# Kernel tuning notes

Hardware: AMD Instinct MI355X
Metric: run time of the kernel (lower is better)

The kernel has to match this reference:

```python
import jax, jax.numpy as jnp
import numpy as np

B, L, D = 4, 2048, 1024
N, K, H = 8, 1, 128
FG, FA = 4096, 2048
SEP = 1792
SOFTCAP = 50.0
EPS = 1e-6
BIG_NEG = -2.3819763e38


def setup_inputs() -> dict:
    key = jax.random.key(0)
    ks = jax.random.split(key, 16)
    def rnd(k, shape, s=0.02):
        return jax.random.normal(k, shape, dtype=jnp.float32) * s
    return {
        "x": rnd(ks[0], (B, L, D), 1.0),
        "positions": jnp.broadcast_to(jnp.arange(L + 1, dtype=jnp.int32), (B, L + 1)),
        "attn_mask": jnp.ones((B, 1, L, L), dtype=bool),
        "separation_idx": SEP,
        "pre_attn_scale": rnd(ks[1], (D,), 0.1),
        "pre_ffw_scale": rnd(ks[2], (D,), 0.1),
        "g_qw": rnd(ks[3], (N, D, H)),
        "g_kvw": rnd(ks[4], (2, K, D, H)),
        "g_ow": rnd(ks[5], (N, H, D)),
        "a_qw": rnd(ks[6], (N, D, H)),
        "a_kvw": rnd(ks[7], (2, K, D, H)),
        "a_ow": rnd(ks[8], (N, H, D)),
        "g_gate": rnd(ks[9], (2, D, FG)),
        "g_lin": rnd(ks[10], (FG, D)),
        "a_gate": rnd(ks[11], (2, D, FA)),
        "a_lin": rnd(ks[12], (FA, D)),
    }


def rms_norm(x, scale):
    var = jnp.mean(jnp.square(x), axis=-1, keepdims=True)
    return x * jax.lax.rsqrt(var + EPS) * (1.0 + scale)


def apply_rope(x, positions, max_wavelength=10_000.0):
    # x: [B,T,n,H], positions: [B,T]
    hd = x.shape[-1]
    frac = 2.0 * jnp.arange(hd // 2, dtype=jnp.float32) / hd
    timescale = max_wavelength ** frac  # [H/2]
    radians = positions.astype(jnp.float32)[:, :, None, None] / timescale  # [B,T,1,H/2]
    sin, cos = jnp.sin(radians), jnp.cos(radians)
    x1, x2 = jnp.split(x, 2, axis=-1)
    return jnp.concatenate([x1 * cos - x2 * sin, x2 * cos + x1 * sin], axis=-1).astype(x.dtype)


def get_qkv(xn, pos, qw, kvw):
    q = jnp.einsum('btd,ndh->btnh', xn, qw)
    q = apply_rope(q, pos) * (H ** -0.5)  # query_pre_attn_norm == 'rsqrt_head_dim'
    k = apply_rope(jnp.einsum('btd,kdh->btkh', xn, kvw[0]), pos)
    v = jnp.einsum('btd,kdh->btkh', xn, kvw[1])
    return q, k, v


def attention(q, k, v, mask):
    b, t, n, h = q.shape
    kk = k.shape[2]
    g = n // kk
    qg = q.reshape(b, t, kk, g, h)
    logits = jnp.einsum('btkgh,bskh->bkgts', qg, k)
    logits = SOFTCAP * jnp.tanh(logits / SOFTCAP)
    logits = jnp.where(mask[:, :, None], logits, BIG_NEG)  # mask [B,1,T,S] -> [B,1,1,T,S]
    probs = jax.nn.softmax(logits.astype(jnp.float32), axis=-1).astype(q.dtype)
    return jnp.einsum('bkgts,bskh->btkgh', probs, v).reshape(b, t, n, h)


def ffn(x, gate, lin):
    h = jax.nn.gelu(jnp.einsum('btd,df->btf', x, gate[0])) * jnp.einsum('btd,df->btf', x, gate[1])
    return jnp.einsum('btf,fd->btd', h, lin)


def process(attn_out, residual, ffw_scale, gate, lin):
    # post_norms=False, dropout=0: out = mlp(norm(attn + res)) + res (per source)
    h = rms_norm(attn_out + residual, ffw_scale)
    return ffn(h, gate, lin) + residual


def reference(x, positions, attn_mask, separation_idx, pre_attn_scale, pre_ffw_scale,
              g_qw, g_kvw, g_ow, a_qw, a_kvw, a_ow, g_gate, g_lin, a_gate, a_lin):
    sep = separation_idx
    x_g, x_a = x[:, :sep], x[:, sep:]
    n_g = rms_norm(x_g, pre_attn_scale)
    n_a = rms_norm(x_a, pre_attn_scale)
    p_g = positions[:, :sep]
    p_a = positions[:, sep + 1:]
    qg, kg, vg = get_qkv(n_g, p_g, g_qw, g_kvw)
    qa, ka, va = get_qkv(n_a, p_a, a_qw, a_kvw)
    q = jnp.concatenate([qg, qa], axis=1)
    k = jnp.concatenate([kg, ka], axis=1)
    v = jnp.concatenate([vg, va], axis=1)
    attn = attention(q, k, v, attn_mask)  # [B,L,N,H]
    go = jnp.einsum('btnh,nhd->btd', attn[:, :sep], g_ow)
    ao = jnp.einsum('btnh,nhd->btd', attn[:, sep:], a_ow)
    out_g = process(go, x_g, pre_ffw_scale, g_gate, g_lin)
    out_a = process(ao, x_a, pre_ffw_scale, a_gate, a_lin)
    return jnp.concatenate([out_g, out_a], axis=1)
```

## Files before the change

### kernel.cpp

```cpp
#include <hip/hip_runtime.h>
#include <hip/hip_bf16.h>
#include <stdint.h>

typedef short s8b __attribute__((ext_vector_type(8)));
typedef float f4 __attribute__((ext_vector_type(4)));
typedef unsigned short u16t;
typedef unsigned int u32t;

#define AS1 __attribute__((address_space(1)))
#define AS3 __attribute__((address_space(3)))
#define DEVFN static __device__ __forceinline__

DEVFN u16t f2b(float f){ union{ __hip_bfloat16 h; u16t u; } c; c.h = __float2bfloat16(f); return c.u; }

DEVFN float geluf(float x){
  float t = 0.7978845608028654f*(x + 0.044715f*x*x*x);
  t = fminf(fmaxf(t, -15.0f), 15.0f);
  float e = __expf(2.0f*t);
  return 0.5f*x*(1.0f + (e-1.0f)*__builtin_amdgcn_rcpf(e+1.0f));
}
DEVFN float softcapf(float x){
  float t = fminf(fmaxf(x*0.02f, -15.0f), 15.0f);
  float e = __expf(2.0f*t);
  return 50.0f*(e-1.0f)*__builtin_amdgcn_rcpf(e+1.0f);
}

__global__ __launch_bounds__(256) void tpack_k(u16t* __restrict__ dst, const float* __restrict__ src,
                                               int ldsrc, int lddst, int rmul, int roff, int prow,
                                               size_t pstride){
  __shared__ float tile[32][33];
  int z = blockIdx.z;
  const float* s = src + (size_t)z*pstride;
  int f0 = blockIdx.x*32, d0 = blockIdx.y*32;
  int t = threadIdx.x, r = t>>5, c = t&31;
  #pragma unroll
  for(int i=0;i<4;i++)
    tile[r + i*8][c] = s[(size_t)(d0 + r + i*8)*ldsrc + f0 + c];
  __syncthreads();
  int rbase = roff + z*prow;
  #pragma unroll
  for(int i=0;i<4;i++){
    int f = f0 + r + i*8;
    dst[(size_t)(f*rmul + rbase)*lddst + d0 + c] = f2b(tile[c][r + i*8]);
  }
}

__global__ __launch_bounds__(256) void rmsnorm_k(const float* __restrict__ x, const float* __restrict__ sc,
                                                 u16t* __restrict__ out){
  int row = blockIdx.x;
  int tid = threadIdx.x;
  const float* xr = x + (size_t)row*1024;
  float4 v = *(const float4*)(xr + tid*4);
  float s = v.x*v.x + v.y*v.y + v.z*v.z + v.w*v.w;
  #pragma unroll
  for(int off=32; off>=1; off>>=1) s += __shfl_down(s, off);
  __shared__ float ws4[4];
  if((tid & 63) == 0) ws4[tid>>6] = s;
  __syncthreads();
  float tot = ws4[0]+ws4[1]+ws4[2]+ws4[3];
  float r = rsqrtf(tot*(1.0f/1024.0f) + 1e-6f);
  float4 scv = *(const float4*)(sc + tid*4);
  u16t o0 = f2b(v.x*r*(1.0f+scv.x)), o1 = f2b(v.y*r*(1.0f+scv.y));
  u16t o2 = f2b(v.z*r*(1.0f+scv.z)), o3 = f2b(v.w*r*(1.0f+scv.w));
  uint2 pk; pk.x = (u32t)o0 | ((u32t)o1<<16); pk.y = (u32t)o2 | ((u32t)o3<<16);
  *(uint2*)(out + (size_t)row*1024 + tid*4) = pk;
}

__global__ __launch_bounds__(256) void rope_k(const float* __restrict__ qkv, u16t* __restrict__ qb,
                                              u16t* __restrict__ kswz, u16t* __restrict__ vrow){
  int row = blockIdx.x;
  int b = row >> 11, t = row & 2047;
  float pos = (float)(t + (t >= 1792 ? 1 : 0));
  const float* src = qkv + (size_t)row*1280;
  size_t kvbase = ((size_t)b*2048 + t)*128;
  int swz = ((t&7)<<3) ^ (((t>>3)&3)<<4);
  for(int idx = threadIdx.x; idx < 704; idx += 256){
    if(idx < 512){
      int n = idx >> 6, i = idx & 63;
      float inv = exp2f((float)i * -0.20762050593046f);
      float sn, cs; sincosf(pos*inv, &sn, &cs);
      float x1 = src[n*128+i], x2 = src[n*128+i+64];
      const float qs = 0.08838834764831845f;
      qb[(size_t)row*1024 + n*128 + i]      = f2b((x1*cs - x2*sn)*qs);
      qb[(size_t)row*1024 + n*128 + i + 64] = f2b((x2*cs + x1*sn)*qs);
    } else if(idx < 576){
      int i = idx - 512;
      float inv = exp2f((float)i * -0.20762050593046f);
      float sn, cs; sincosf(pos*inv, &sn, &cs);
      float x1 = src[1024+i], x2 = src[1024+i+64];
      kswz[kvbase + (i ^ swz)]        = f2b(x1*cs - x2*sn);
      kswz[kvbase + ((i+64) ^ swz)]   = f2b(x2*cs + x1*sn);
    } else {
      int h = idx - 576;
      vrow[kvbase + h] = f2b(src[1152+h]);
    }
  }
}

__global__ __launch_bounds__(256) void vt_pack_k(const u16t* __restrict__ vrow, u16t* __restrict__ vtswz){
  int blk = blockIdx.x;
  int b = blk >> 5, kt = blk & 31;
  int tid = threadIdx.x;
  const u16t* src = vrow + ((size_t)b*2048 + kt*64)*128;
  #pragma unroll
  for(int it=0; it<4; ++it){
    int o = it*2048 + tid*8;
    int d = o >> 6, kg = o & 63;
    u16t tmp[8];
    #pragma unroll
    for(int j=0;j<8;j++) tmp[j] = src[(size_t)(kg+j)*128 + d];
    *(uint4*)&vtswz[((size_t)b*128 + d)*2048 + kt*64 + (kg ^ ((d&7)<<3))] = *(const uint4*)tmp;
  }
}

struct GemmArgs {
  const u16t* A; int lda;
  const u16t* Bg; const u16t* Ba;
  int K; int ntN; int mode; int amap; int omap; int ep;
  float* outf; u16t* outb; int ldo;
  const float* res;
};

__global__ __launch_bounds__(256) void gemm_k(GemmArgs g){
  __shared__ __align__(16) u16t As[2*128*32];
  __shared__ __align__(16) u16t Bs[2*128*32];
  int bid = blockIdx.x;
  int mt = bid / g.ntN, nt = bid % g.ntN;
  int c0 = mt*128, g0;
  const u16t* B;
  if(g.mode == 0){
    g0 = c0;
    B = ((mt & 15) < 14) ? g.Bg : g.Ba;
  } else if(g.mode == 1){
    int bb = mt/14, t = (mt - bb*14)*128;
    g0 = bb*2048 + t; B = g.Bg;
  } else {
    int bb = mt>>1, t = 1792 + (mt&1)*128;
    g0 = bb*2048 + t; B = g.Bg;
  }
  int arow = g.amap ? g0 : c0;
  int orow = g.omap ? g0 : c0;
  int tid = threadIdx.x, lane = tid & 63, w = tid >> 6, l15 = lane & 15, lg = lane >> 4;
  int wr = w >> 1, wc = w & 1;

  int gsrc = ((tid&3) ^ ((tid>>3)&3))*8;
  const u16t* Ap = g.A + (size_t)(arow + (tid>>2))*g.lda + gsrc;
  const u16t* Bp = B   + (size_t)(nt*128 + (tid>>2))*g.K + gsrc;
  size_t lda64 = (size_t)64*g.lda, ldb64 = (size_t)64*g.K;
  u32t le = tid*8;

  int xr = (lg ^ ((l15>>1)&3))*8;
  int aoff[4], boff[4];
  #pragma unroll
  for(int mi=0;mi<4;mi++) aoff[mi] = (wr*64 + mi*16 + l15)*32 + xr;
  #pragma unroll
  for(int ni=0;ni<4;ni++) boff[ni] = (wc*64 + ni*16 + l15)*32 + xr;

  f4 acc[4][4];
  #pragma unroll
  for(int mi=0;mi<4;mi++)
    #pragma unroll
    for(int ni=0;ni<4;ni++){ f4 z = {0.0f,0.0f,0.0f,0.0f}; acc[mi][ni]=z; }

  auto stagef = [&](int buf, int k0){
    u16t* a = As + buf*4096;
    u16t* b = Bs + buf*4096;
    __builtin_amdgcn_global_load_lds((const AS1 u32t*)(Ap + k0),          (AS3 u32t*)&a[le],        16,0,0);
    __builtin_amdgcn_global_load_lds((const AS1 u32t*)(Ap + k0 + lda64),  (AS3 u32t*)&a[le + 2048], 16,0,0);
    __builtin_amdgcn_global_load_lds((const AS1 u32t*)(Bp + k0),          (AS3 u32t*)&b[le],        16,0,0);
    __builtin_amdgcn_global_load_lds((const AS1 u32t*)(Bp + k0 + ldb64),  (AS3 u32t*)&b[le + 2048], 16,0,0);
  };

  stagef(0, 0);
  __syncthreads();
  int cur = 0;
  for(int k0=0; k0 < g.K; k0 += 32){
    if(k0 + 32 < g.K) stagef(cur^1, k0+32);
    const u16t* as = As + cur*4096;
    const u16t* bs = Bs + cur*4096;
    s8b af[4], bf[4];
    #pragma unroll
    for(int mi=0;mi<4;mi++) af[mi] = *(const s8b*)&as[aoff[mi]];
    #pragma unroll
    for(int ni=0;ni<4;ni++) bf[ni] = *(const s8b*)&bs[boff[ni]];
    #pragma unroll
    for(int mi=0;mi<4;mi++)
      #pragma unroll
      for(int ni=0;ni<4;ni++)
        acc[mi][ni] = __builtin_amdgcn_mfma_f32_16x16x32_bf16(af[mi], bf[ni], acc[mi][ni], 0,0,0);
    __syncthreads();
    cur ^= 1;
  }

  #pragma unroll
  for(int mi=0;mi<4;mi++){
    #pragma unroll
    for(int ni=0;ni<4;ni++){
      int rowb = wr*64 + mi*16 + lg*4;
      int col = nt*128 + wc*64 + ni*16 + l15;
      #pragma unroll
      for(int r=0;r<4;r++){
        float v = acc[mi][ni][r];
        size_t ro = (size_t)(orow + rowb + r);
        if(g.ep == 0){
          g.outf[ro*(size_t)g.ldo + col] = v;
        } else if(g.ep == 1){
          g.outf[ro*(size_t)g.ldo + col] = v + g.res[ro*1024 + col];
        } else {
          float other = __shfl_xor(v, 1);
          if((lane & 1) == 0){
            g.outb[ro*(size_t)g.ldo + (col>>1)] = f2b(geluf(v)*other);
          }
        }
      }
    }
  }
}

__global__ __launch_bounds__(512, 2) void gemm256_k(const u16t* __restrict__ A,
                                                    const u16t* __restrict__ Bw,
                                                    u16t* __restrict__ outb){
  __shared__ __align__(16) u16t LDS[65536];
  int bid = blockIdx.x;
  int j = bid >> 3;
  int nt = (bid & 7)*4 + (j & 3);
  int mt = j >> 2;
  int bb = mt / 7;
  int g0 = bb*2048 + (mt - bb*7)*256;
  int orow0 = mt*256;
  int tid = threadIdx.x, lane = tid & 63, w = tid >> 6, l15 = lane & 15, lg = lane >> 4;
  int wr = w >> 2, wc = w & 3;

  int cg = ((tid&7) ^ ((tid>>3)&7))*8;
  const u16t* aSrc = A  + (size_t)(g0 + (tid>>3))*1024 + cg;
  const u16t* bSrc = Bw + (size_t)(nt*256 + (tid>>3))*1024 + cg;
  u16t* ldsA = &LDS[w*512 + (lane&63)*8];
  u16t* ldsB = &LDS[32768 + w*512 + (lane&63)*8];

  auto STAGE_A = [&](int kt, int uh){
    if(kt >= 16) return;
    const u16t* s0 = aSrc + (size_t)(uh*128)*1024 + kt*64;
    u16t* d = ldsA + (kt&1)*16384 + uh*8192;
    __builtin_amdgcn_global_load_lds((const AS1 u32t*)s0,            (AS3 u32t*)d,          16,0,0);
    __builtin_amdgcn_global_load_lds((const AS1 u32t*)(s0 + 65536),  (AS3 u32t*)(d + 4096), 16,0,0);
  };
  auto STAGE_B = [&](int kt, int uh){
    if(kt >= 16) return;
    const u16t* s0 = bSrc + (size_t)(uh*128)*1024 + kt*64;
    u16t* d = ldsB + (kt&1)*16384 + uh*8192;
    __builtin_amdgcn_global_load_lds((const AS1 u32t*)s0,            (AS3 u32t*)d,          16,0,0);
    __builtin_amdgcn_global_load_lds((const AS1 u32t*)(s0 + 65536),  (AS3 u32t*)(d + 4096), 16,0,0);
  };

  int px0 = ((lg)     ^ (l15&7))*8;
  int px1 = ((4 + lg) ^ (l15&7))*8;
  int aRow = (wr*128 + l15)*64;
  int bRow = (wc*64  + l15)*64;

  f4 acc[8][4];
  #pragma unroll
  for(int m=0;m<8;m++)
    #pragma unroll
    for(int n=0;n<4;n++){ f4 z = {0.0f,0.0f,0.0f,0.0f}; acc[m][n]=z; }
  s8b afr[4][2], bfr[4][2];

  auto READ_A = [&](int s, int mh){
    const u16t* base = &LDS[s*16384 + aRow + mh*4096];
    #pragma unroll
    for(int m=0;m<4;m++){
      afr[m][0] = *(const s8b*)(base + m*1024 + px0);
      afr[m][1] = *(const s8b*)(base + m*1024 + px1);
    }
  };
  auto READ_B = [&](int s, int nh){
    const u16t* base = &LDS[32768 + s*16384 + bRow + nh*2048];
    #pragma unroll
    for(int n=0;n<2;n++){
      bfr[nh*2+n][0] = *(const s8b*)(base + n*1024 + px0);
      bfr[nh*2+n][1] = *(const s8b*)(base + n*1024 + px1);
    }
  };

  #define MFMAQ(mh, nh)                                                              \
    __builtin_amdgcn_s_barrier();                                                    \
    asm volatile("s_waitcnt lgkmcnt(0)" ::: "memory");                               \
    __builtin_amdgcn_sched_barrier(0);                                               \
    __builtin_amdgcn_s_setprio(1);                                                   \
    _Pragma("unroll")                                                                \
    for(int m=0;m<4;m++)                                                             \
      _Pragma("unroll")                                                              \
      for(int n=0;n<2;n++)                                                           \
        _Pragma("unroll")                                                            \
        for(int kk=0;kk<2;kk++)                                                      \
          acc[(mh)*4+m][(nh)*2+n] = __builtin_amdgcn_mfma_f32_16x16x32_bf16(         \
              afr[m][kk], bfr[(nh)*2+n][kk], acc[(mh)*4+m][(nh)*2+n], 0,0,0);        \
    __builtin_amdgcn_s_setprio(0);                                                   \
    __builtin_amdgcn_sched_barrier(0);

  STAGE_A(0,0); STAGE_A(0,1); STAGE_B(0,0); STAGE_B(0,1);
  STAGE_A(1,0); STAGE_A(1,1);
  asm volatile("s_waitcnt vmcnt(4)" ::: "memory");
  __builtin_amdgcn_s_barrier();

  for(int it2=0; it2<8; ++it2){
    int t = it2*2;
    READ_B(0,0); READ_A(0,0); STAGE_B(t+1, 0);
    MFMAQ(0,0)
    __builtin_amdgcn_s_barrier();
    READ_B(0,1); STAGE_B(t+1, 1);
    MFMAQ(0,1)
    __builtin_amdgcn_s_barrier();
    READ_A(0,1); STAGE_A(t+2, 0);
    MFMAQ(1,0)
    __builtin_amdgcn_s_barrier();
    STAGE_A(t+2, 1);
    MFMAQ(1,1)
    if(it2==7) asm volatile("s_waitcnt vmcnt(0)" ::: "memory");
    else       asm volatile("s_waitcnt vmcnt(4)" ::: "memory");
    __builtin_amdgcn_s_barrier();
    READ_B(1,0); READ_A(1,0); STAGE_B(t+2, 0);
    MFMAQ(0,0)
    __builtin_amdgcn_s_barrier();
    READ_B(1,1); STAGE_B(t+2, 1);
    MFMAQ(0,1)
    __builtin_amdgcn_s_barrier();
    READ_A(1,1); STAGE_A(t+3, 0);
    MFMAQ(1,0)
    __builtin_amdgcn_s_barrier();
    STAGE_A(t+3, 1);
    MFMAQ(1,1)
    if(it2==7) asm volatile("s_waitcnt vmcnt(0)" ::: "memory");
    else       asm volatile("s_waitcnt vmcnt(4)" ::: "memory");
    __builtin_amdgcn_s_barrier();
  }
  #undef MFMAQ

  #pragma unroll
  for(int mg=0;mg<8;mg++){
    #pragma unroll
    for(int n=0;n<4;n++){
      int rowb = wr*128 + mg*16 + lg*4;
      int col = nt*256 + wc*64 + n*16 + l15;
      #pragma unroll
      for(int r=0;r<4;r++){
        float v = acc[mg][n][r];
        float other = __shfl_xor(v, 1);
        if((lane & 1) == 0){
          size_t ro = (size_t)(orow0 + rowb + r);
          outb[ro*4096 + (col>>1)] = f2b(geluf(v)*other);
        }
      }
    }
  }
}

__global__ __launch_bounds__(256) void attn_k(const u16t* __restrict__ qb, const u16t* __restrict__ kswz,
                                              const u16t* __restrict__ vtswz, u16t* __restrict__ attnb){
  __shared__ __align__(16) u16t Ks[2*64*128];
  __shared__ __align__(16) u16t Vt[2*128*64];
  __shared__ __align__(16) u16t Ps[4*16*72];
  int bid = blockIdx.x;
  int qt = bid & 31, n = (bid>>5)&7, b = bid>>8;
  int tid = threadIdx.x, lane = tid&63, w = tid>>6, l15 = lane&15, lg = lane>>4;
  int q0 = qt*64 + w*16;

  s8b qf[4];
  const u16t* qrow = qb + ((size_t)(b*2048 + q0 + l15)*8 + n)*128;
  #pragma unroll
  for(int kc=0;kc<4;kc++) qf[kc] = *(const s8b*)(qrow + kc*32 + lg*8);

  float lsum[4];
  f4 oacc[8];
  #pragma unroll
  for(int r=0;r<4;r++) lsum[r] = 0.0f;
  #pragma unroll
  for(int db=0;db<8;db++){ f4 z = {0.0f,0.0f,0.0f,0.0f}; oacc[db]=z; }

  const u16t* kbase  = kswz  + (size_t)b*2048*128;
  const u16t* vtbase = vtswz + (size_t)b*128*2048;
  u16t* psw = Ps + w*1152;

  auto stage = [&](int buf, int st){
    const u16t* kt  = kbase  + (size_t)st*64*128;
    const u16t* vtb = vtbase + st*64;
    u16t* kd = Ks + buf*8192;
    u16t* vd = Vt + buf*8192;
    #pragma unroll
    for(int it=0; it<4; ++it){
      int e = it*2048 + tid*8;
      __builtin_amdgcn_global_load_lds((const AS1 u32t*)(kt + e), (AS3 u32t*)&kd[e], 16,0,0);
    }
    #pragma unroll
    for(int it=0; it<4; ++it){
      int e = it*2048 + tid*8;
      int d = e >> 6, ko = e & 63;
      __builtin_amdgcn_global_load_lds((const AS1 u32t*)(vtb + (size_t)d*2048 + ko), (AS3 u32t*)&vd[e], 16,0,0);
    }
  };

  stage(0, 0);
  __syncthreads();
  int cur = 0;
  for(int st=0; st<32; ++st){
    if(st < 31) stage(cur^1, st+1);
    const u16t* ks = Ks + cur*8192;
    const u16t* vs = Vt + cur*8192;

    f4 sf[4];
    #pragma unroll
    for(int kb=0;kb<4;kb++){ f4 z = {0.0f,0.0f,0.0f,0.0f}; sf[kb]=z; }
    #pragma unroll
    for(int kb=0;kb<4;kb++){
      int key = kb*16 + l15;
      int swz = ((key&7)<<3) ^ (((key>>3)&3)<<4);
      #pragma unroll
      for(int kc=0;kc<4;kc++){
        s8b kf = *(const s8b*)&ks[key*128 + ((kc*32 + lg*8) ^ swz)];
        sf[kb] = __builtin_amdgcn_mfma_f32_16x16x32_bf16(qf[kc], kf, sf[kb], 0,0,0);
      }
    }
    #pragma unroll
    for(int r=0;r<4;r++){
      int prow = lg*4 + r;
      #pragma unroll
      for(int kb=0;kb<4;kb++){
        float pv = __expf(softcapf(sf[kb][r]));
        lsum[r] += pv;
        psw[prow*72 + kb*16 + l15] = f2b(pv);
      }
    }
    #pragma unroll
    for(int kc2=0;kc2<2;kc2++){
      s8b pa = *(const s8b*)&psw[l15*72 + kc2*32 + lg*8];
      int koff = (kc2*32 + lg*8) ^ ((l15&7)<<3);
      #pragma unroll
      for(int db=0;db<8;db++){
        s8b vf = *(const s8b*)&vs[(db*16 + l15)*64 + koff];
        oacc[db] = __builtin_amdgcn_mfma_f32_16x16x32_bf16(pa, vf, oacc[db], 0,0,0);
      }
    }
    __syncthreads();
    cur ^= 1;
  }

  float linv[4];
  #pragma unroll
  for(int r=0;r<4;r++){
    float s = lsum[r];
    #pragma unroll
    for(int off=1; off<16; off<<=1) s += __shfl_xor(s, off);
    linv[r] = 1.0f / s;
  }

  #pragma unroll
  for(int db=0;db<8;db++){
    #pragma unroll
    for(int r=0;r<4;r++){
      int qrowi = q0 + lg*4 + r;
      int d = db*16 + l15;
      attnb[(size_t)(b*2048 + qrowi)*1024 + n*128 + d] = f2b(oacc[db][r] * linv[r]);
    }
  }
}

extern "C" void kernel_launch(void* const* d_in, const int* in_sizes, int n_in,
                              void* d_out, int out_size, void* d_ws, size_t ws_size,
                              hipStream_t stream){
  const float* x        = (const float*)d_in[0];
  const float* pre_attn = (const float*)d_in[4];
  const float* pre_ffw  = (const float*)d_in[5];
  const float* g_qw  = (const float*)d_in[6];
  const float* g_kvw = (const float*)d_in[7];
  const float* g_ow  = (const float*)d_in[8];
  const float* a_qw  = (const float*)d_in[9];
  const float* a_kvw = (const float*)d_in[10];
  const float* a_ow  = (const float*)d_in[11];
  const float* g_gate= (const float*)d_in[12];
  const float* g_lin = (const float*)d_in[13];
  const float* a_gate= (const float*)d_in[14];
  const float* a_lin = (const float*)d_in[15];
  float* out = (float*)d_out;
  (void)in_sizes; (void)n_in; (void)out_size; (void)ws_size;

  char* wsp = (char*)d_ws; size_t off = 0;
  auto alloc = [&](size_t b){ void* p = wsp + off; off += (b + 255) & ~(size_t)255; return p; };
  u16t* wqkv_g = (u16t*)alloc((size_t)1280*1024*2);
  u16t* wqkv_a = (u16t*)alloc((size_t)1280*1024*2);
  u16t* wo_g   = (u16t*)alloc((size_t)1024*1024*2);
  u16t* wo_a   = (u16t*)alloc((size_t)1024*1024*2);
  u16t* wg_g   = (u16t*)alloc((size_t)8192*1024*2);
  u16t* wg_a   = (u16t*)alloc((size_t)4096*1024*2);
  u16t* wl_g   = (u16t*)alloc((size_t)1024*4096*2);
  u16t* wl_a   = (u16t*)alloc((size_t)1024*2048*2);
  u16t* xn     = (u16t*)alloc((size_t)8192*1024*2);
  u16t* xn2    = xn;
  char* big    = (char*)alloc((size_t)7168*4096*2);
  float* qkv   = (float*)big;
  float* t1    = (float*)big;
  u16t* hid_g  = (u16t*)big;
  u16t* qb     = (u16t*)alloc((size_t)8192*1024*2);
  u16t* kswz   = (u16t*)alloc((size_t)4*2048*128*2);
  u16t* vrow   = (u16t*)alloc((size_t)4*2048*128*2);
  u16t* vtswz  = (u16t*)alloc((size_t)4*128*2048*2);
  u16t* attnb  = (u16t*)alloc((size_t)8192*1024*2);
  u16t* hid_a  = (u16t*)alloc((size_t)1024*2048*2);

  tpack_k<<<dim3(4,32,8),256,0,stream>>>(wqkv_g, g_qw, 128, 1024, 1, 0, 128, 131072);
  tpack_k<<<dim3(4,32,1),256,0,stream>>>(wqkv_g, g_kvw, 128, 1024, 1, 1024, 0, 0);
  tpack_k<<<dim3(4,32,1),256,0,stream>>>(wqkv_g, g_kvw + 131072, 128, 1024, 1, 1152, 0, 0);
  tpack_k<<<dim3(4,32,8),256,0,stream>>>(wqkv_a, a_qw, 128, 1024, 1, 0, 128, 131072);
  tpack_k<<<dim3(4,32,1),256,0,stream>>>(wqkv_a, a_kvw, 128, 1024, 1, 1024, 0, 0);
  tpack_k<<<dim3(4,32,1),256,0,stream>>>(wqkv_a, a_kvw + 131072, 128, 1024, 1, 1152, 0, 0);
  tpack_k<<<dim3(32,32,1),256,0,stream>>>(wo_g, g_ow, 1024, 1024, 1, 0, 0, 0);
  tpack_k<<<dim3(32,32,1),256,0,stream>>>(wo_a, a_ow, 1024, 1024, 1, 0, 0, 0);
  tpack_k<<<dim3(128,32,2),256,0,stream>>>(wg_g, g_gate, 4096, 1024, 2, 0, 1, (size_t)1024*4096);
  tpack_k<<<dim3(64,32,2),256,0,stream>>>(wg_a, a_gate, 2048, 1024, 2, 0, 1, (size_t)1024*2048);
  tpack_k<<<dim3(32,128,1),256,0,stream>>>(wl_g, g_lin, 1024, 4096, 1, 0, 0, 0);
  tpack_k<<<dim3(32,64,1),256,0,stream>>>(wl_a, a_lin, 1024, 2048, 1, 0, 0, 0);

  rmsnorm_k<<<8192,256,0,stream>>>(x, pre_attn, xn);

  { GemmArgs ga = {xn, 1024, wqkv_g, wqkv_a, 1024, 10, 0,0,0, 0, qkv, nullptr, 1280, nullptr};
    gemm_k<<<64*10,256,0,stream>>>(ga); }
  rope_k<<<8192,256,0,stream>>>(qkv, qb, kswz, vrow);
  vt_pack_k<<<128,256,0,stream>>>(vrow, vtswz);
  attn_k<<<1024,256,0,stream>>>(qb, kswz, vtswz, attnb);
  { GemmArgs ga = {attnb, 1024, wo_g, wo_a, 1024, 8, 0,0,0, 1, t1, nullptr, 1024, x};
    gemm_k<<<64*8,256,0,stream>>>(ga); }
  rmsnorm_k<<<8192,256,0,stream>>>(t1, pre_ffw, xn2);
  gemm256_k<<<896,512,0,stream>>>(xn2, wg_g, hid_g);
  { GemmArgs ga = {xn2, 1024, wg_a, nullptr, 1024, 32, 2,1,0, 3, nullptr, hid_a, 2048, nullptr};
    gemm_k<<<8*32,256,0,stream>>>(ga); }
  { GemmArgs ga = {hid_g, 4096, wl_g, nullptr, 4096, 8, 1,0,1, 1, out, nullptr, 1024, x};
    gemm_k<<<56*8,256,0,stream>>>(ga); }
  { GemmArgs ga = {hid_a, 2048, wl_a, nullptr, 2048, 8, 2,0,1, 1, out, nullptr, 1024, x};
    gemm_k<<<8*8,256,0,stream>>>(ga); }
}
```

Measured before the change: 813.2 us.

## Merge audio gate GEMM into gemm256 launch and cheapen softcap/gelu math

The separate gemm_k launch for the audio FFN gate projection is folded into the 256-tile gemm256_k kernel as 64 extra blocks, each selecting its own weight, output pointer and leading dimension. This removes one launch and lets the small audio GEMM fill the tail of the large text GEMM's grid. The GELU and softcap-exp functions are rewritten with exp2 intrinsics, dropping the clamps and the separate exp call on the attention probabilities. Without the clamps, overflow behavior for large inputs relies on exp2 saturating to inf and rcp returning zero.

```diff
diff --git a/kernel.cpp b/kernel.cpp
--- a/kernel.cpp
+++ b/kernel.cpp
@@ -14,15 +14,15 @@
 DEVFN u16t f2b(float f){ union{ __hip_bfloat16 h; u16t u; } c; c.h = __float2bfloat16(f); return c.u; }
 
 DEVFN float geluf(float x){
-  float t = 0.7978845608028654f*(x + 0.044715f*x*x*x);
-  t = fminf(fmaxf(t, -15.0f), 15.0f);
-  float e = __expf(2.0f*t);
-  return 0.5f*x*(1.0f + (e-1.0f)*__builtin_amdgcn_rcpf(e+1.0f));
-}
-DEVFN float softcapf(float x){
-  float t = fminf(fmaxf(x*0.02f, -15.0f), 15.0f);
-  float e = __expf(2.0f*t);
-  return 50.0f*(e-1.0f)*__builtin_amdgcn_rcpf(e+1.0f);
+  float u = x*(0.7978845608028654f + 0.03567740813636141f*x*x);
+  float e = __builtin_amdgcn_exp2f(u*2.8853900817779268f);
+  float th = 1.0f - 2.0f*__builtin_amdgcn_rcpf(e + 1.0f);
+  return 0.5f*x*(1.0f + th);
+}
+DEVFN float softexpf(float s){
+  float e = __builtin_amdgcn_exp2f(s*0.05770780163555853f);
+  float th = 1.0f - 2.0f*__builtin_amdgcn_rcpf(e + 1.0f);
+  return __builtin_amdgcn_exp2f(th*72.13475204444817f);
 }
 
 __global__ __launch_bounds__(256) void tpack_k(u16t* __restrict__ dst, const float* __restrict__ src,
@@ -218,16 +218,27 @@
 }
 
 __global__ __launch_bounds__(512, 2) void gemm256_k(const u16t* __restrict__ A,
-                                                    const u16t* __restrict__ Bw,
-                                                    u16t* __restrict__ outb){
+                                                    const u16t* __restrict__ Bg,
+                                                    const u16t* __restrict__ Ba,
+                                                    u16t* __restrict__ outg,
+                                                    u16t* __restrict__ outa){
   __shared__ __align__(16) u16t LDS[65536];
   int bid = blockIdx.x;
-  int j = bid >> 3;
-  int nt = (bid & 7)*4 + (j & 3);
-  int mt = j >> 2;
-  int bb = mt / 7;
-  int g0 = bb*2048 + (mt - bb*7)*256;
-  int orow0 = mt*256;
+  int mt, nt, g0, orow0, ldo;
+  const u16t* Bw; u16t* outb;
+  if(bid < 896){
+    int j = bid >> 3;
+    nt = (bid & 7)*4 + (j & 3);
+    mt = j >> 2;
+    int bb = mt / 7;
+    g0 = bb*2048 + (mt - bb*7)*256;
+    orow0 = mt*256; Bw = Bg; outb = outg; ldo = 4096;
+  } else {
+    int idx = bid - 896;
+    mt = idx >> 4; nt = idx & 15;
+    g0 = mt*2048 + 1792;
+    orow0 = mt*256; Bw = Ba; outb = outa; ldo = 2048;
+  }
   int tid = threadIdx.x, lane = tid & 63, w = tid >> 6, l15 = lane & 15, lg = lane >> 4;
   int wr = w >> 2, wc = w & 3;
 
@@ -347,7 +358,7 @@
         float other = __shfl_xor(v, 1);
         if((lane & 1) == 0){
           size_t ro = (size_t)(orow0 + rowb + r);
-          outb[ro*4096 + (col>>1)] = f2b(geluf(v)*other);
+          outb[ro*(size_t)ldo + (col>>1)] = f2b(geluf(v)*other);
         }
       }
     }
@@ -424,7 +435,7 @@
       int prow = lg*4 + r;
       #pragma unroll
       for(int kb=0;kb<4;kb++){
-        float pv = __expf(softcapf(sf[kb][r]));
+        float pv = softexpf(sf[kb][r]);
         lsum[r] += pv;
         psw[prow*72 + kb*16 + l15] = f2b(pv);
       }
@@ -528,9 +539,7 @@
   { GemmArgs ga = {attnb, 1024, wo_g, wo_a, 1024, 8, 0,0,0, 1, t1, nullptr, 1024, x};
     gemm_k<<<64*8,256,0,stream>>>(ga); }
   rmsnorm_k<<<8192,256,0,stream>>>(t1, pre_ffw, xn2);
-  gemm256_k<<<896,512,0,stream>>>(xn2, wg_g, hid_g);
-  { GemmArgs ga = {xn2, 1024, wg_a, nullptr, 1024, 32, 2,1,0, 3, nullptr, hid_a, 2048, nullptr};
-    gemm_k<<<8*32,256,0,stream>>>(ga); }
+  gemm256_k<<<960,512,0,stream>>>(xn2, wg_g, wg_a, hid_g, hid_a);
   { GemmArgs ga = {hid_g, 4096, wl_g, nullptr, 4096, 8, 1,0,1, 1, out, nullptr, 1024, x};
     gemm_k<<<56*8,256,0,stream>>>(ga); }
   { GemmArgs ga = {hid_a, 2048, wl_a, nullptr, 2048, 8, 2,0,1, 1, out, nullptr, 1024, x};
```

After: 780.8 us. 1.04x faster.
